# Optimization experiments

Measured on AMD Instinct MI355X. Metric: run time of the kernel, lower is better.

Reference implementation:

```python
import jax, jax.numpy as jnp
import numpy as np

N = 50000; E = 800000; IN = 128; OUT = 64; ED = 16; H = 4
NEG_SLOPE = 0.2


def adaptive_avg_pool1d(v, L):
    """torch F.adaptive_avg_pool1d on a 1-D vector v -> length L (static slices)."""
    S = v.shape[0]
    return jnp.stack([v[(i * S) // L: -((-(i + 1) * S) // L)].mean() for i in range(L)])


def gat_conv(x, edge_index, edge_attr, W_gat, att_src, att_dst, W_edge, att_edge, b_gat):
    """PyG GATConv(heads=H, concat=False, edge_dim=ED), eval mode (no dropout)."""
    n = x.shape[0]
    h, c = att_src.shape
    xs = (x @ W_gat).reshape(n, h, c)                       # [N,H,C]
    a_src = jnp.einsum('nhc,hc->nh', xs, att_src)           # [N,H]
    a_dst = jnp.einsum('nhc,hc->nh', xs, att_dst)           # [N,H]
    e = (edge_attr @ W_edge).reshape(-1, h, c)              # [E,H,C]
    a_edge = jnp.einsum('ehc,hc->eh', e, att_edge)          # [E,H]
    src, dst = edge_index[0], edge_index[1]
    alpha = a_src[src] + a_dst[dst] + a_edge                # [E,H]
    alpha = jax.nn.leaky_relu(alpha, NEG_SLOPE)
    # segment softmax over incoming edges of each destination node
    amax = jax.ops.segment_max(alpha, dst, num_segments=n)  # [N,H]
    ex = jnp.exp(alpha - amax[dst])
    denom = jax.ops.segment_sum(ex, dst, num_segments=n)
    alpha = ex / (denom[dst] + 1e-16)
    msg = xs[src] * alpha[:, :, None]                       # [E,H,C]
    out = jax.ops.segment_sum(msg, dst, num_segments=n)     # [N,H,C]
    return out.mean(axis=1) + b_gat                         # concat=False -> head mean


def setup_inputs():
    key = jax.random.key(0)
    ks = jax.random.split(key, 16)
    p = lambda k, s: jax.random.normal(k, s, dtype=jnp.float32) * 0.05
    return {
        'x': jax.random.normal(ks[0], (N, IN), dtype=jnp.float32),
        'edge_index': jax.random.randint(ks[1], (2, E), 0, N),
        'edge_attr': jax.random.normal(ks[2], (E, ED), dtype=jnp.float32),
        'quality_raw': jax.random.uniform(ks[3], (E, 4), dtype=jnp.float32),
        'network_state': jax.random.uniform(ks[4], (8,), dtype=jnp.float32),
        'W_gat': p(ks[5], (IN, H * OUT)),
        'att_src': p(ks[6], (H, OUT)),
        'att_dst': p(ks[7], (H, OUT)),
        'W_edge': p(ks[8], (ED, H * OUT)),
        'att_edge': p(ks[9], (H, OUT)),
        'b_gat': jnp.zeros((OUT,), jnp.float32),
        'W_q1': p(ks[10], (4, ED // 2)),
        'b_q1': jnp.zeros((ED // 2,), jnp.float32),
        'W_q2': p(ks[11], (ED // 2, ED)),
        'b_q2': jnp.zeros((ED,), jnp.float32),
        'W_c': p(ks[12], (OUT + ED, OUT)),
        'b_c': jnp.zeros((OUT,), jnp.float32),
    }


def reference(x, edge_index, edge_attr, quality_raw, network_state,
              W_gat, att_src, att_dst, W_edge, att_edge, b_gat,
              W_q1, b_q1, W_q2, b_q2, W_c, b_c):
    # vectorized path-quality encoder (replaces per-edge python loop)
    q = jax.nn.relu(quality_raw @ W_q1 + b_q1) @ W_q2 + b_q2      # [E,ED]
    enhanced_edge_attr = edge_attr + q
    x_conv = gat_conv(x, edge_index, enhanced_edge_attr,
                      W_gat, att_src, att_dst, W_edge, att_edge, b_gat)  # [N,OUT]
    cf = adaptive_avg_pool1d(network_state, ED)                    # [ED]
    cf = jnp.broadcast_to(cf, (x.shape[0], ED))                    # [N,ED]
    h = jnp.concatenate([x_conv, cf], axis=-1)                     # [N,OUT+ED]
    return jax.nn.relu(h @ W_c + b_c)                              # [N,OUT]
```

## Files before the change

### kernel.cpp

```cpp
#include <hip/hip_runtime.h>
#include <hip/hip_bf16.h>

#define NN 50000
#define EE 800000
#define NEG 0.2f
#define NSH 16
#define NS (NN*NSH)
#define NSB2 196
#define NGB 1563
#define NDB 782

using u32 = unsigned int;
typedef short short4v __attribute__((ext_vector_type(4)));
typedef float f32x4 __attribute__((ext_vector_type(4)));
typedef unsigned int u32x4 __attribute__((ext_vector_type(4)));

__device__ __forceinline__ unsigned short f2bf(float f){
  u32 b = __float_as_uint(f);
  b += 0x7FFFu + ((b >> 16) & 1u);
  return (unsigned short)(b >> 16);
}

__global__ __launch_bounds__(256) void k_pre_all(
        const float* __restrict__ Wg, const float* __restrict__ W_c,
        const float* __restrict__ W_edge, const float* __restrict__ att_edge,
        const float* __restrict__ b_c, const float* __restrict__ ns,
        const float* __restrict__ b_gat,
        const float* __restrict__ att_src, const float* __restrict__ att_dst,
        unsigned short* __restrict__ WzB, float* __restrict__ Wt,
        float* __restrict__ cvec, uint2* __restrict__ avp){
  int bid = blockIdx.x, tid = threadIdx.x;
  if (bid < 128){
    __shared__ float sWg[256];
    __shared__ float sWc[64*64];
    sWg[tid] = Wg[bid*256 + tid];
    for (int i = tid; i < 4096; i += 256) sWc[i] = W_c[i];
    __syncthreads();
    int h = tid >> 6, j = tid & 63;
    float s = 0.f;
    #pragma unroll 8
    for (int c = 0; c < 64; c++) s += sWg[h*64 + c] * sWc[c*64 + j];
    int t = tid >> 4, lr = tid & 15;
    int ks = bid >> 4, lg = (bid >> 2) & 3, q = bid & 3;
    int l = lg*16 + lr;
    WzB[(((t*8 + ks)*64 + l) << 2) + q] = f2bf(s);
  } else if (bid == 128){
    if (tid < 64){
      int d = tid >> 2, h = tid & 3;
      float s = 0.f;
      for (int c = 0; c < 64; c++) s += W_edge[d*256 + h*64 + c] * att_edge[h*64 + c];
      Wt[d*4 + h] = s;
    } else if (tid < 128){
      int j = tid - 64;
      float s = b_c[j];
      for (int d = 0; d < 16; d++) s += ns[d >> 1] * W_c[(64 + d)*64 + j];
      for (int c = 0; c < 64; c++) s += b_gat[c] * W_c[c*64 + j];
      cvec[j] = s;
    }
  } else {
    __shared__ float sav2[1024];
    for (int i = tid; i < 1024; i += 256){
      int k = i >> 3, o = i & 7, h = o & 3;
      const float* att = (o < 4) ? att_src : att_dst;
      float s = 0.f;
      for (int c = 0; c < 64; c++) s += Wg[k*256 + h*64 + c] * att[h*64 + c];
      sav2[i] = s;
    }
    __syncthreads();
    if (tid < 64){
      int l = tid, lg = l >> 4, lr = l & 15;
      for (int ks = 0; ks < 8; ks++){
        unsigned int h0, h1, h2, h3;
        int kb = ks*16 + lg*4;
        h0 = (lr < 8) ? f2bf(sav2[(kb+0)*8 + lr]) : 0u;
        h1 = (lr < 8) ? f2bf(sav2[(kb+1)*8 + lr]) : 0u;
        h2 = (lr < 8) ? f2bf(sav2[(kb+2)*8 + lr]) : 0u;
        h3 = (lr < 8) ? f2bf(sav2[(kb+3)*8 + lr]) : 0u;
        uint2 u; u.x = h0 | (h1 << 16); u.y = h2 | (h3 << 16);
        avp[ks*64 + l] = u;
      }
    }
  }
}

__global__ __launch_bounds__(256) void k_main(const float* __restrict__ x,
        const unsigned short* __restrict__ WzB, const uint2* __restrict__ avp,
        const int* __restrict__ dsts,
        __hip_bfloat16* __restrict__ zs,
        float* __restrict__ a_src, float* __restrict__ a_dst,
        u32* __restrict__ deg16, unsigned short* __restrict__ rank){
  __shared__ alignas(16) char ldsu[17408];
  int tid = threadIdx.x;
  int bid = blockIdx.x;

  if ((bid % 3) == 1){
    int g = bid / 3;
    int gi = g*256 + tid;
    if (gi*4 < EE){
      int shard = g & (NSH-1);
      int4 d4 = *(const int4*)(dsts + (size_t)gi*4);
      u32 r0 = atomicAdd(&deg16[((size_t)(u32)d4.x << 4) | shard], 1u);
      u32 r1 = atomicAdd(&deg16[((size_t)(u32)d4.y << 4) | shard], 1u);
      u32 r2 = atomicAdd(&deg16[((size_t)(u32)d4.z << 4) | shard], 1u);
      u32 r3 = atomicAdd(&deg16[((size_t)(u32)d4.w << 4) | shard], 1u);
      uint2 pk;
      pk.x = (r0 & 0xffffu) | (r1 << 16);
      pk.y = (r2 & 0xffffu) | (r3 << 16);
      *(uint2*)(rank + (size_t)gi*4) = pk;
    }
    return;
  }

  int gb = bid - (bid + 2)/3;
  int w = tid >> 6, l = tid & 63;
  int lr = l & 15, lg = l >> 4;
  int rw = w >> 1, ch = w & 1;
  int nb = gb*32;
  int n0 = nb + rw*16;

  float* xsl = (float*)ldsu;
  __hip_bfloat16* ztp = (__hip_bfloat16*)ldsu;

  {
    float4 stg[4];
    #pragma unroll
    for (int i = 0; i < 4; i++){
      int s = w*256 + i*64 + l;
      int r = s >> 5, c = s & 31;
      int row = nb + r; if (row >= NN) row = NN - 1;
      stg[i] = *(const float4*)(x + (size_t)row*128 + c*4);
    }
    #pragma unroll
    for (int i = 0; i < 4; i++){
      int s = w*256 + i*64 + l;
      *(float4*)(xsl + s*4) = stg[i];
    }
  }
  __syncthreads();

  short4v afr[8];
  #pragma unroll
  for (int ks = 0; ks < 8; ks++){
    float4 xa = *(const float4*)(xsl + ((rw*16 + lr)*128 + ks*16 + lg*4));
    short4v a;
    a[0] = (short)f2bf(xa.x); a[1] = (short)f2bf(xa.y);
    a[2] = (short)f2bf(xa.z); a[3] = (short)f2bf(xa.w);
    afr[ks] = a;
  }
  if (ch == 0){
    f32x4 cad = {0.f, 0.f, 0.f, 0.f};
    #pragma unroll
    for (int ks = 0; ks < 8; ks++){
      short4v b = __builtin_bit_cast(short4v, avp[ks*64 + l]);
      cad = __builtin_amdgcn_mfma_f32_16x16x16bf16_1k(afr[ks], b, cad, 0, 0, 0);
    }
    #pragma unroll
    for (int r = 0; r < 4; r++){
      int n = n0 + lg*4 + r;
      if (n < NN){
        if (lr < 4)      a_src[(size_t)n*4 + lr]       = cad[r];
        else if (lr < 8) a_dst[(size_t)n*4 + (lr - 4)] = cad[r];
      }
    }
  }
  __syncthreads();

  #pragma unroll 4
  for (int t8 = 0; t8 < 8; t8++){
    int t = ch*8 + t8;
    f32x4 c = {0.f, 0.f, 0.f, 0.f};
    #pragma unroll
    for (int ks = 0; ks < 8; ks++){
      short4v b = *(const short4v*)(WzB + (((t*8 + ks)*64 + l) << 2));
      c = __builtin_amdgcn_mfma_f32_16x16x16bf16_1k(afr[ks], b, c, 0, 0, 0);
    }
    #pragma unroll
    for (int r = 0; r < 4; r++)
      ztp[((w*16) + lg*4 + r)*136 + t8*16 + lr] = __float2bfloat16(c[r]);
  }
  #pragma unroll
  for (int i = 0; i < 4; i++){
    int f = i*64 + l;
    int row = f >> 4, c16 = f & 15;
    int n = n0 + row;
    if (n < NN)
      *(uint4*)(zs + (size_t)n*256 + ch*128 + c16*8) = *(const uint4*)&ztp[(w*16 + row)*136 + c16*8];
  }
}

__global__ __launch_bounds__(1024) void k_scan1(const u32* __restrict__ deg16,
                                                u32* __restrict__ offs16, u32* __restrict__ bsum){
  __shared__ u32 sd[1024];
  int t = threadIdx.x;
  size_t base = (size_t)blockIdx.x*4096 + (size_t)t*4;
  u32x4 v = {0u,0u,0u,0u};
  if (base < NS) v = *(const u32x4*)(deg16 + base);
  u32 o1 = v.x, o2 = o1 + v.y, o3 = o2 + v.z;
  u32 tsum = o3 + v.w;
  sd[t] = tsum; __syncthreads();
  for (int off = 1; off < 1024; off <<= 1){
    u32 u = (t >= off) ? sd[t-off] : 0u;
    __syncthreads();
    sd[t] += u;
    __syncthreads();
  }
  u32 excl = sd[t] - tsum;
  if (base < NS){
    u32x4 o = {excl, excl + o1, excl + o2, excl + o3};
    *(u32x4*)(offs16 + base) = o;
  }
  if (t == 1023) bsum[blockIdx.x] = sd[1023];
}

__global__ __launch_bounds__(1024) void k_scan2(u32* __restrict__ offs16,
                                                const u32* __restrict__ bsum){
  __shared__ u32 sd[1024];
  int b = blockIdx.x, t = threadIdx.x;
  sd[t] = (t < b) ? bsum[t] : 0u;
  __syncthreads();
  #pragma unroll
  for (int off = 512; off; off >>= 1){
    if (t < off) sd[t] += sd[t + off];
    __syncthreads();
  }
  u32 p = sd[0];
  size_t base = (size_t)b*4096 + (size_t)t*4;
  if (base < NS){
    u32x4 o = *(u32x4*)(offs16 + base);
    o.x += p; o.y += p; o.z += p; o.w += p;
    *(u32x4*)(offs16 + base) = o;
  }
  if (b == 0 && t == 0) offs16[NS] = EE;
}

__global__ __launch_bounds__(256) void k_edge(const float* __restrict__ qraw,
        const float* __restrict__ eattr, const int* __restrict__ eidx,
        const float* __restrict__ Wq1, const float* __restrict__ bq1,
        const float* __restrict__ Wq2, const float* __restrict__ bq2,
        const float* __restrict__ Wt,
        const float* __restrict__ a_src,
        const u32* __restrict__ offs16, const unsigned short* __restrict__ rank,
        uint4* __restrict__ csr){
  __shared__ float sWq1[32], sbq1[8], sWq2[128], sbq2[16], sWt[64];
  int tid = threadIdx.x;
  if (tid < 32) sWq1[tid] = Wq1[tid];
  else if (tid < 40)  sbq1[tid-32]  = bq1[tid-32];
  else if (tid < 168) sWq2[tid-40]  = Wq2[tid-40];
  else if (tid < 184) sbq2[tid-168] = bq2[tid-168];
  else if (tid < 248) sWt[tid-184]  = Wt[tid-184];
  __syncthreads();
  int e = blockIdx.x*256 + tid;
  if (e >= EE) return;
  int shard = (blockIdx.x >> 2) & (NSH-1);

  float4 qr = *(const float4*)(qraw + (size_t)e*4);
  float t1[8];
  #pragma unroll
  for (int j = 0; j < 8; j++){
    float s = sbq1[j] + qr.x*sWq1[j] + qr.y*sWq1[8+j] + qr.z*sWq1[16+j] + qr.w*sWq1[24+j];
    t1[j] = fmaxf(s, 0.f);
  }
  float ae[4] = {0.f,0.f,0.f,0.f};
  const float* ea = eattr + (size_t)e*16;
  #pragma unroll
  for (int d = 0; d < 16; d++){
    float q = sbq2[d];
    #pragma unroll
    for (int j = 0; j < 8; j++) q += t1[j]*sWq2[j*16 + d];
    float v = ea[d] + q;
    #pragma unroll
    for (int h = 0; h < 4; h++) ae[h] += v * sWt[d*4 + h];
  }
  int src = eidx[e], dst = eidx[EE + e];
  float4 as4 = *(const float4*)(a_src + (size_t)src*4);
  u32 pk0 = (u32)f2bf(as4.x + ae[0]);
  u32 pk1 = (u32)f2bf(as4.y + ae[1]);
  u32 pk2 = (u32)f2bf(as4.z + ae[2]);
  u32 pk3 = (u32)f2bf(as4.w + ae[3]);
  u32 pos = offs16[((size_t)(u32)dst << 4) | shard] + (u32)rank[e];
  uint4 q;
  q.x = (u32)src;
  q.y = pk0 | (pk1 << 16);
  q.z = pk2 | (pk3 << 16);
  q.w = 0u;
  csr[pos] = q;
}

__global__ __launch_bounds__(256) void k_agg(const __hip_bfloat16* __restrict__ zs,
        const uint4* __restrict__ csr, const u32* __restrict__ offs16,
        const float* __restrict__ a_dst,
        const float* __restrict__ cvec, float* __restrict__ out){
  int tid = threadIdx.x;
  int w = tid >> 6, lane = tid & 63;
  int half = lane >> 5, sl = lane & 31;
  int n = blockIdx.x*8 + w*2 + half;
  int h = sl >> 3, c8 = sl & 7;
  u32 p0 = offs16[(size_t)n << 4], p1 = offs16[((size_t)n << 4) + 16];
  float adv = a_dst[((size_t)n << 2) + h];
  int sh = (h & 1) ? 0 : 16;
  u32 lb = (u32)(h*128 + c8*16);
  const char* zb = (const char*)zs;
  float d = 0.f;
  float a0=0.f,a1=0.f,a2=0.f,a3=0.f,a4=0.f,a5=0.f,a6=0.f,a7=0.f;
  u32 p = p0;
  for (; p + 4 <= p1; p += 4){
    uint4 q0 = csr[p+0], q1 = csr[p+1], q2 = csr[p+2], q3 = csr[p+3];
    u32 s0 = q0.x, s1 = q1.x, s2 = q2.x, s3 = q3.x;
    u32 w0p = (h < 2) ? q0.y : q0.z,  w1p = (h < 2) ? q1.y : q1.z;
    u32 w2p = (h < 2) ? q2.y : q2.z,  w3p = (h < 2) ? q3.y : q3.z;
    uint4 v0 = *(const uint4*)(zb + ((s0 << 9) + lb));
    uint4 v1 = *(const uint4*)(zb + ((s1 << 9) + lb));
    uint4 v2 = *(const uint4*)(zb + ((s2 << 9) + lb));
    uint4 v3 = *(const uint4*)(zb + ((s3 << 9) + lb));
    float al0 = __uint_as_float((w0p << sh) & 0xffff0000u) + adv;
    float al1 = __uint_as_float((w1p << sh) & 0xffff0000u) + adv;
    float al2 = __uint_as_float((w2p << sh) & 0xffff0000u) + adv;
    float al3 = __uint_as_float((w3p << sh) & 0xffff0000u) + adv;
    al0 = fmaxf(al0, 0.f) + NEG*fminf(al0, 0.f);
    al1 = fmaxf(al1, 0.f) + NEG*fminf(al1, 0.f);
    al2 = fmaxf(al2, 0.f) + NEG*fminf(al2, 0.f);
    al3 = fmaxf(al3, 0.f) + NEG*fminf(al3, 0.f);
    float w0 = __expf(al0), w1 = __expf(al1), w2 = __expf(al2), w3 = __expf(al3);
    a0 += w0*__uint_as_float(v0.x << 16)         + w1*__uint_as_float(v1.x << 16)
        + w2*__uint_as_float(v2.x << 16)         + w3*__uint_as_float(v3.x << 16);
    a1 += w0*__uint_as_float(v0.x & 0xffff0000u) + w1*__uint_as_float(v1.x & 0xffff0000u)
        + w2*__uint_as_float(v2.x & 0xffff0000u) + w3*__uint_as_float(v3.x & 0xffff0000u);
    a2 += w0*__uint_as_float(v0.y << 16)         + w1*__uint_as_float(v1.y << 16)
        + w2*__uint_as_float(v2.y << 16)         + w3*__uint_as_float(v3.y << 16);
    a3 += w0*__uint_as_float(v0.y & 0xffff0000u) + w1*__uint_as_float(v1.y & 0xffff0000u)
        + w2*__uint_as_float(v2.y & 0xffff0000u) + w3*__uint_as_float(v3.y & 0xffff0000u);
    a4 += w0*__uint_as_float(v0.z << 16)         + w1*__uint_as_float(v1.z << 16)
        + w2*__uint_as_float(v2.z << 16)         + w3*__uint_as_float(v3.z << 16);
    a5 += w0*__uint_as_float(v0.z & 0xffff0000u) + w1*__uint_as_float(v1.z & 0xffff0000u)
        + w2*__uint_as_float(v2.z & 0xffff0000u) + w3*__uint_as_float(v3.z & 0xffff0000u);
    a6 += w0*__uint_as_float(v0.w << 16)         + w1*__uint_as_float(v1.w << 16)
        + w2*__uint_as_float(v2.w << 16)         + w3*__uint_as_float(v3.w << 16);
    a7 += w0*__uint_as_float(v0.w & 0xffff0000u) + w1*__uint_as_float(v1.w & 0xffff0000u)
        + w2*__uint_as_float(v2.w & 0xffff0000u) + w3*__uint_as_float(v3.w & 0xffff0000u);
    d  += (w0 + w1) + (w2 + w3);
  }
  for (; p < p1; p++){
    uint4 q0 = csr[p];
    u32 wp = (h < 2) ? q0.y : q0.z;
    float al = __uint_as_float((wp << sh) & 0xffff0000u) + adv;
    al = fmaxf(al, 0.f) + NEG*fminf(al, 0.f);
    float w0 = __expf(al);
    uint4 v0 = *(const uint4*)(zb + ((q0.x << 9) + lb));
    a0 += w0*__uint_as_float(v0.x << 16);
    a1 += w0*__uint_as_float(v0.x & 0xffff0000u);
    a2 += w0*__uint_as_float(v0.y << 16);
    a3 += w0*__uint_as_float(v0.y & 0xffff0000u);
    a4 += w0*__uint_as_float(v0.z << 16);
    a5 += w0*__uint_as_float(v0.z & 0xffff0000u);
    a6 += w0*__uint_as_float(v0.w << 16);
    a7 += w0*__uint_as_float(v0.w & 0xffff0000u);
    d  += w0;
  }
  float inv = (d > 0.f) ? 0.25f / d : 0.f;
  a0 *= inv; a1 *= inv; a2 *= inv; a3 *= inv;
  a4 *= inv; a5 *= inv; a6 *= inv; a7 *= inv;
  a0 += __shfl_xor(a0, 8);  a1 += __shfl_xor(a1, 8);
  a2 += __shfl_xor(a2, 8);  a3 += __shfl_xor(a3, 8);
  a4 += __shfl_xor(a4, 8);  a5 += __shfl_xor(a5, 8);
  a6 += __shfl_xor(a6, 8);  a7 += __shfl_xor(a7, 8);
  a0 += __shfl_xor(a0, 16); a1 += __shfl_xor(a1, 16);
  a2 += __shfl_xor(a2, 16); a3 += __shfl_xor(a3, 16);
  a4 += __shfl_xor(a4, 16); a5 += __shfl_xor(a5, 16);
  a6 += __shfl_xor(a6, 16); a7 += __shfl_xor(a7, 16);
  if (h == 0){
    const float* cv = cvec + c8*8;
    float4 o0, o1v;
    o0.x  = fmaxf(a0 + cv[0], 0.f);
    o0.y  = fmaxf(a1 + cv[1], 0.f);
    o0.z  = fmaxf(a2 + cv[2], 0.f);
    o0.w  = fmaxf(a3 + cv[3], 0.f);
    o1v.x = fmaxf(a4 + cv[4], 0.f);
    o1v.y = fmaxf(a5 + cv[5], 0.f);
    o1v.z = fmaxf(a6 + cv[6], 0.f);
    o1v.w = fmaxf(a7 + cv[7], 0.f);
    float* op = out + (size_t)n*64 + c8*8;
    *(float4*)op = o0;
    *(float4*)(op + 4) = o1v;
  }
}

extern "C" void kernel_launch(void* const* d_in, const int* in_sizes, int n_in,
                              void* d_out, int out_size, void* d_ws, size_t ws_size,
                              hipStream_t stream){
  const float* x       = (const float*)d_in[0];
  const int*   eidx    = (const int*)d_in[1];
  const float* eattr   = (const float*)d_in[2];
  const float* qraw    = (const float*)d_in[3];
  const float* ns      = (const float*)d_in[4];
  const float* Wg      = (const float*)d_in[5];
  const float* att_src = (const float*)d_in[6];
  const float* att_dst = (const float*)d_in[7];
  const float* W_edge  = (const float*)d_in[8];
  const float* att_edge= (const float*)d_in[9];
  const float* b_gat   = (const float*)d_in[10];
  const float* Wq1     = (const float*)d_in[11];
  const float* bq1     = (const float*)d_in[12];
  const float* Wq2     = (const float*)d_in[13];
  const float* bq2     = (const float*)d_in[14];
  const float* W_c     = (const float*)d_in[15];
  const float* b_c     = (const float*)d_in[16];
  float* out = (float*)d_out;

  char* ws = (char*)d_ws;
  __hip_bfloat16* zs = (__hip_bfloat16*)ws;
  uint4* csr      = (uint4*)(ws + 25600000);
  u32* deg16      = (u32*)(ws + 25600000);
  u32* offs16     = (u32*)(ws + 38400000);
  float* a_src    = (float*)(ws + 41600064);
  float* a_dst    = (float*)(ws + 42400064);
  unsigned short* rank = (unsigned short*)(ws + 43200064);
  u32* bsum       = (u32*)(ws + 44800064);
  unsigned short* WzB = (unsigned short*)(ws + 44804160);
  uint2* avp      = (uint2*)(ws + 44869696);
  float* Wt       = (float*)(ws + 44873792);
  float* cvec     = (float*)(ws + 44874048);

  hipMemsetAsync(deg16, 0, (size_t)NS*4, stream);

  k_pre_all<<<130,      256, 0, stream>>>(Wg, W_c, W_edge, att_edge, b_c, ns, b_gat,
                                          att_src, att_dst, WzB, Wt, cvec, avp);
  k_main   <<<NGB+NDB,  256, 0, stream>>>(x, WzB, avp, eidx + EE, zs, a_src, a_dst,
                                          deg16, rank);
  k_scan1  <<<NSB2,    1024, 0, stream>>>(deg16, offs16, bsum);
  k_scan2  <<<NSB2,    1024, 0, stream>>>(offs16, bsum);
  k_edge   <<<3125,     256, 0, stream>>>(qraw, eattr, eidx, Wq1, bq1, Wq2, bq2, Wt,
                                          a_src, offs16, rank, csr);
  k_agg    <<<6250,     256, 0, stream>>>(zs, csr, offs16, a_dst, cvec, out);
}
```

Baseline: 167.5 us.

## Halve degree shards and fold deg-buffer zeroing into precompute kernel

Reduces the per-node shard count for degree counting from 16 to 8, halving the size of the degree/offset arrays and the work of both scan kernels. Replaces the separate memset with extra blocks in the precompute kernel that zero the degree buffer, removing one launch. Also hoists the index, a_src and offset loads in the edge kernel ahead of the MLP math to overlap latency. Fewer shards raise atomic contention per counter.

After: 159.0 us. 5.1% less time.

```diff
diff --git a/kernel.cpp b/kernel.cpp
--- a/kernel.cpp
+++ b/kernel.cpp
@@ -4,9 +4,10 @@
 #define NN 50000
 #define EE 800000
 #define NEG 0.2f
-#define NSH 16
+#define NSH 8
 #define NS (NN*NSH)
-#define NSB2 196
+#define NSB2 98
+#define NZB 98
 #define NGB 1563
 #define NDB 782
 
@@ -28,7 +29,8 @@
         const float* __restrict__ b_gat,
         const float* __restrict__ att_src, const float* __restrict__ att_dst,
         unsigned short* __restrict__ WzB, float* __restrict__ Wt,
-        float* __restrict__ cvec, uint2* __restrict__ avp){
+        float* __restrict__ cvec, uint2* __restrict__ avp,
+        u32* __restrict__ deg8){
   int bid = blockIdx.x, tid = threadIdx.x;
   if (bid < 128){
     __shared__ float sWg[256];
@@ -57,7 +59,7 @@
       for (int c = 0; c < 64; c++) s += b_gat[c] * W_c[c*64 + j];
       cvec[j] = s;
     }
-  } else {
+  } else if (bid == 129){
     __shared__ float sav2[1024];
     for (int i = tid; i < 1024; i += 256){
       int k = i >> 3, o = i & 7, h = o & 3;
@@ -80,6 +82,14 @@
         avp[ks*64 + l] = u;
       }
     }
+  } else {
+    u32x4 z = {0u,0u,0u,0u};
+    int slot0 = ((bid - 130)*256 + tid)*4;
+    #pragma unroll
+    for (int i = 0; i < 4; i++){
+      int slot = slot0 + i;
+      if (slot*4 < NS) *(u32x4*)(deg8 + slot*4) = z;
+    }
   }
 }
 
@@ -88,7 +98,7 @@
         const int* __restrict__ dsts,
         __hip_bfloat16* __restrict__ zs,
         float* __restrict__ a_src, float* __restrict__ a_dst,
-        u32* __restrict__ deg16, unsigned short* __restrict__ rank){
+        u32* __restrict__ deg8, unsigned short* __restrict__ rank){
   __shared__ alignas(16) char ldsu[17408];
   int tid = threadIdx.x;
   int bid = blockIdx.x;
@@ -99,10 +109,10 @@
     if (gi*4 < EE){
       int shard = g & (NSH-1);
       int4 d4 = *(const int4*)(dsts + (size_t)gi*4);
-      u32 r0 = atomicAdd(&deg16[((size_t)(u32)d4.x << 4) | shard], 1u);
-      u32 r1 = atomicAdd(&deg16[((size_t)(u32)d4.y << 4) | shard], 1u);
-      u32 r2 = atomicAdd(&deg16[((size_t)(u32)d4.z << 4) | shard], 1u);
-      u32 r3 = atomicAdd(&deg16[((size_t)(u32)d4.w << 4) | shard], 1u);
+      u32 r0 = atomicAdd(&deg8[((size_t)(u32)d4.x << 3) | shard], 1u);
+      u32 r1 = atomicAdd(&deg8[((size_t)(u32)d4.y << 3) | shard], 1u);
+      u32 r2 = atomicAdd(&deg8[((size_t)(u32)d4.z << 3) | shard], 1u);
+      u32 r3 = atomicAdd(&deg8[((size_t)(u32)d4.w << 3) | shard], 1u);
       uint2 pk;
       pk.x = (r0 & 0xffffu) | (r1 << 16);
       pk.y = (r2 & 0xffffu) | (r3 << 16);
@@ -188,13 +198,13 @@
   }
 }
 
-__global__ __launch_bounds__(1024) void k_scan1(const u32* __restrict__ deg16,
-                                                u32* __restrict__ offs16, u32* __restrict__ bsum){
+__global__ __launch_bounds__(1024) void k_scan1(const u32* __restrict__ deg8,
+                                                u32* __restrict__ offs8, u32* __restrict__ bsum){
   __shared__ u32 sd[1024];
   int t = threadIdx.x;
   size_t base = (size_t)blockIdx.x*4096 + (size_t)t*4;
   u32x4 v = {0u,0u,0u,0u};
-  if (base < NS) v = *(const u32x4*)(deg16 + base);
+  if (base < NS) v = *(const u32x4*)(deg8 + base);
   u32 o1 = v.x, o2 = o1 + v.y, o3 = o2 + v.z;
   u32 tsum = o3 + v.w;
   sd[t] = tsum; __syncthreads();
@@ -207,12 +217,12 @@
   u32 excl = sd[t] - tsum;
   if (base < NS){
     u32x4 o = {excl, excl + o1, excl + o2, excl + o3};
-    *(u32x4*)(offs16 + base) = o;
+    *(u32x4*)(offs8 + base) = o;
   }
   if (t == 1023) bsum[blockIdx.x] = sd[1023];
 }
 
-__global__ __launch_bounds__(1024) void k_scan2(u32* __restrict__ offs16,
+__global__ __launch_bounds__(1024) void k_scan2(u32* __restrict__ offs8,
                                                 const u32* __restrict__ bsum){
   __shared__ u32 sd[1024];
   int b = blockIdx.x, t = threadIdx.x;
@@ -226,11 +236,11 @@
   u32 p = sd[0];
   size_t base = (size_t)b*4096 + (size_t)t*4;
   if (base < NS){
-    u32x4 o = *(u32x4*)(offs16 + base);
+    u32x4 o = *(u32x4*)(offs8 + base);
     o.x += p; o.y += p; o.z += p; o.w += p;
-    *(u32x4*)(offs16 + base) = o;
-  }
-  if (b == 0 && t == 0) offs16[NS] = EE;
+    *(u32x4*)(offs8 + base) = o;
+  }
+  if (b == 0 && t == 0) offs8[NS] = EE;
 }
 
 __global__ __launch_bounds__(256) void k_edge(const float* __restrict__ qraw,
@@ -239,7 +249,7 @@
         const float* __restrict__ Wq2, const float* __restrict__ bq2,
         const float* __restrict__ Wt,
         const float* __restrict__ a_src,
-        const u32* __restrict__ offs16, const unsigned short* __restrict__ rank,
+        const u32* __restrict__ offs8, const unsigned short* __restrict__ rank,
         uint4* __restrict__ csr){
   __shared__ float sWq1[32], sbq1[8], sWq2[128], sbq2[16], sWt[64];
   int tid = threadIdx.x;
@@ -253,7 +263,12 @@
   if (e >= EE) return;
   int shard = (blockIdx.x >> 2) & (NSH-1);
 
+  int src = eidx[e], dst = eidx[EE + e];
+  u32 rk = (u32)rank[e];
   float4 qr = *(const float4*)(qraw + (size_t)e*4);
+  float4 as4 = *(const float4*)(a_src + (size_t)src*4);
+  u32 base = offs8[((size_t)(u32)dst << 3) | shard];
+
   float t1[8];
   #pragma unroll
   for (int j = 0; j < 8; j++){
@@ -271,13 +286,11 @@
     #pragma unroll
     for (int h = 0; h < 4; h++) ae[h] += v * sWt[d*4 + h];
   }
-  int src = eidx[e], dst = eidx[EE + e];
-  float4 as4 = *(const float4*)(a_src + (size_t)src*4);
   u32 pk0 = (u32)f2bf(as4.x + ae[0]);
   u32 pk1 = (u32)f2bf(as4.y + ae[1]);
   u32 pk2 = (u32)f2bf(as4.z + ae[2]);
   u32 pk3 = (u32)f2bf(as4.w + ae[3]);
-  u32 pos = offs16[((size_t)(u32)dst << 4) | shard] + (u32)rank[e];
+  u32 pos = base + rk;
   uint4 q;
   q.x = (u32)src;
   q.y = pk0 | (pk1 << 16);
@@ -287,7 +300,7 @@
 }
 
 __global__ __launch_bounds__(256) void k_agg(const __hip_bfloat16* __restrict__ zs,
-        const uint4* __restrict__ csr, const u32* __restrict__ offs16,
+        const uint4* __restrict__ csr, const u32* __restrict__ offs8,
         const float* __restrict__ a_dst,
         const float* __restrict__ cvec, float* __restrict__ out){
   int tid = threadIdx.x;
@@ -295,7 +308,7 @@
   int half = lane >> 5, sl = lane & 31;
   int n = blockIdx.x*8 + w*2 + half;
   int h = sl >> 3, c8 = sl & 7;
-  u32 p0 = offs16[(size_t)n << 4], p1 = offs16[((size_t)n << 4) + 16];
+  u32 p0 = offs8[(size_t)n << 3], p1 = offs8[((size_t)n << 3) + 8];
   float adv = a_dst[((size_t)n << 2) + h];
   int sh = (h & 1) ? 0 : 16;
   u32 lb = (u32)(h*128 + c8*16);
@@ -409,8 +422,8 @@
   char* ws = (char*)d_ws;
   __hip_bfloat16* zs = (__hip_bfloat16*)ws;
   uint4* csr      = (uint4*)(ws + 25600000);
-  u32* deg16      = (u32*)(ws + 25600000);
-  u32* offs16     = (u32*)(ws + 38400000);
+  u32* deg8       = (u32*)(ws + 25600000);
+  u32* offs8      = (u32*)(ws + 38400000);
   float* a_src    = (float*)(ws + 41600064);
   float* a_dst    = (float*)(ws + 42400064);
   unsigned short* rank = (unsigned short*)(ws + 43200064);
@@ -420,15 +433,13 @@
   float* Wt       = (float*)(ws + 44873792);
   float* cvec     = (float*)(ws + 44874048);
 
-  hipMemsetAsync(deg16, 0, (size_t)NS*4, stream);
-
-  k_pre_all<<<130,      256, 0, stream>>>(Wg, W_c, W_edge, att_edge, b_c, ns, b_gat,
-                                          att_src, att_dst, WzB, Wt, cvec, avp);
+  k_pre_all<<<130+NZB,  256, 0, stream>>>(Wg, W_c, W_edge, att_edge, b_c, ns, b_gat,
+                                          att_src, att_dst, WzB, Wt, cvec, avp, deg8);
   k_main   <<<NGB+NDB,  256, 0, stream>>>(x, WzB, avp, eidx + EE, zs, a_src, a_dst,
-                                          deg16, rank);
-  k_scan1  <<<NSB2,    1024, 0, stream>>>(deg16, offs16, bsum);
-  k_scan2  <<<NSB2,    1024, 0, stream>>>(offs16, bsum);
+                                          deg8, rank);
+  k_scan1  <<<NSB2,    1024, 0, stream>>>(deg8, offs8, bsum);
+  k_scan2  <<<NSB2,    1024, 0, stream>>>(offs8, bsum);
   k_edge   <<<3125,     256, 0, stream>>>(qraw, eattr, eidx, Wq1, bq1, Wq2, bq2, Wt,
-                                          a_src, offs16, rank, csr);
-  k_agg    <<<6250,     256, 0, stream>>>(zs, csr, offs16, a_dst, cvec, out);
-}
+                                          a_src, offs8, rank, csr);
+  k_agg    <<<6250,     256, 0, stream>>>(zs, csr, offs8, a_dst, cvec, out);
+}
```
